# Optimization experiments

Measured on AMD Instinct MI355X. Metric: run time of the kernel, lower is better.

## Reference

```python
import jax, jax.numpy as jnp
import numpy as np

N = 8192          # total nodes in batch
D_IN = 64         # input feature dim
D_H = 64          # hidden dim
D_OUT = 10        # num classes
B = 64            # number of graphs (idx in [0, B))
NUM_ITERS = 5     # power iterations for rs-pool
VALUE_ALPHA = 1.0
EPS = 0.0         # GIN eps (train_eps=False)


def setup_inputs() -> dict:
    key = jax.random.key(0)
    ks = jax.random.split(key, 8)
    x_in = jax.random.normal(ks[0], (N, D_IN), dtype=jnp.float32)
    a = (jax.random.uniform(ks[1], (N, N)) < 0.005).astype(jnp.float32)
    adj = jnp.maximum(a, a.T)
    idx = (jnp.arange(N) // (N // B)).astype(jnp.int32)  # 64 graphs x 128 nodes
    s1 = 1.0 / np.sqrt(D_IN)
    s2 = 1.0 / np.sqrt(D_H)
    W1 = jax.random.uniform(ks[2], (D_IN, D_H), minval=-s1, maxval=s1, dtype=jnp.float32)
    b1 = jax.random.uniform(ks[3], (D_H,), minval=-s1, maxval=s1, dtype=jnp.float32)
    W2 = jax.random.uniform(ks[4], (D_H, D_H), minval=-s2, maxval=s2, dtype=jnp.float32)
    b2 = jax.random.uniform(ks[5], (D_H,), minval=-s2, maxval=s2, dtype=jnp.float32)
    Wl = jax.random.uniform(ks[6], (D_H, D_OUT), minval=-s2, maxval=s2, dtype=jnp.float32)
    bl = jax.random.uniform(ks[7], (D_OUT,), minval=-s2, maxval=s2, dtype=jnp.float32)
    return {"x_in": x_in, "adj": adj, "idx": idx,
            "W1": W1, "b1": b1, "W2": W2, "b2": b2, "Wl": Wl, "bl": bl}


def reference(x_in, adj, idx, W1, b1, W2, b2, Wl, bl):
    n = adj.shape[0]
    A = adj + jnp.eye(n, dtype=adj.dtype)  # self-loops added in forward
    # GINConv: aggregate (A@x + eps*x) then linear + ReLU
    h = jax.nn.relu((A @ x_in + EPS * x_in) @ W1 + b1)   # [N, D_H]
    h = jax.nn.relu((A @ h + EPS * h) @ W2 + b2)         # [N, D_H]

    seg = lambda v: jax.ops.segment_sum(v, idx, num_segments=B)

    # rs-pool: batched power iteration for dominant right singular vector per graph
    vec = seg(h)                                                   # [B, D_H]
    vec = vec / (jnp.linalg.norm(vec, axis=1, keepdims=True) + 1e-8)
    for _ in range(NUM_ITERS):
        y = jnp.sum(h * vec[idx], axis=1, keepdims=True)           # X_g @ v_g, per node
        vec = seg(y * h)                                           # X_g^T (X_g v_g)
        vec = vec / (jnp.linalg.norm(vec, axis=1, keepdims=True) + 1e-8)
    y = jnp.sum(h * vec[idx], axis=1)                              # [N]
    sv = jnp.sqrt(seg(y * y))                                      # ||X_g v_g|| per graph [B]
    pooled = vec * (sv / VALUE_ALPHA)[:, None]                     # [B, D_H]

    out = pooled @ Wl + bl                                         # [B, D_OUT]
    return jax.nn.log_softmax(out, axis=1)
```

## Files before the change

### kernel.cpp

```cpp
#include <hip/hip_runtime.h>
#include <math.h>

#define NN 8192
#define DH 64
#define DOUT 10
#define NG 64
#define NPG 128
#define NITER 5
#define CAP 192
#define CAPW 96

__global__ __launch_bounds__(256) void gin1_fused(
    const float* __restrict__ adj, const float* __restrict__ x,
    const float* __restrict__ W, const float* __restrict__ bias,
    float* __restrict__ h, unsigned short* __restrict__ eidx,
    int* __restrict__ counts)
{
    __shared__ float sW[DH * DH];
    __shared__ float sAccP[4][DH];
    __shared__ float sAccR[DH];
    __shared__ unsigned short sIdx[4][CAPW];
    __shared__ int sCnt[4];

    for (int t = threadIdx.x; t < DH * DH; t += 256) sW[t] = W[t];

    const int wave = threadIdx.x >> 6;
    const int lane = threadIdx.x & 63;
    const int row  = blockIdx.x;

    const float* arow = adj + (size_t)row * NN + wave * 2048;
    const unsigned long long lt = (lane == 63) ? 0x7FFFFFFFFFFFFFFFull
                                               : ((1ull << lane) - 1ull);
    int ec = 0;
    #pragma unroll
    for (int j0 = 0; j0 < 2048; j0 += 256) {
        float4 a4 = *reinterpret_cast<const float4*>(arow + j0 + lane * 4);
        unsigned long long m0 = __ballot(a4.x != 0.0f);
        unsigned long long m1 = __ballot(a4.y != 0.0f);
        unsigned long long m2 = __ballot(a4.z != 0.0f);
        unsigned long long m3 = __ballot(a4.w != 0.0f);
        int pre = __popcll(m0 & lt) + __popcll(m1 & lt) +
                  __popcll(m2 & lt) + __popcll(m3 & lt);
        int pos = ec + pre;
        int jb = wave * 2048 + j0 + 4 * lane;
        if ((m0 >> lane) & 1) sIdx[wave][pos++] = (unsigned short)(jb + 0);
        if ((m1 >> lane) & 1) sIdx[wave][pos++] = (unsigned short)(jb + 1);
        if ((m2 >> lane) & 1) sIdx[wave][pos++] = (unsigned short)(jb + 2);
        if ((m3 >> lane) & 1) sIdx[wave][pos++] = (unsigned short)(jb + 3);
        ec += __popcll(m0) + __popcll(m1) + __popcll(m2) + __popcll(m3);
    }
    if (lane == 0) sCnt[wave] = ec;
    __syncthreads();

    int c0 = sCnt[0], c1 = sCnt[1], c2 = sCnt[2], c3 = sCnt[3];
    int off = (wave > 0 ? c0 : 0) + (wave > 1 ? c1 : 0) + (wave > 2 ? c2 : 0);
    for (int e = lane; e < ec; e += 64)
        eidx[(size_t)row * CAP + off + e] = sIdx[wave][e];
    if (threadIdx.x == 0) counts[row] = c0 + c1 + c2 + c3;

    float acc = (wave == 0) ? x[row * DH + lane] : 0.0f;
    #pragma unroll 4
    for (int e = 0; e < ec; ++e) {
        int j = sIdx[wave][e];
        acc += x[j * DH + lane];
    }
    sAccP[wave][lane] = acc;
    __syncthreads();

    if (wave == 0) {
        float a = sAccP[0][lane] + sAccP[1][lane] + sAccP[2][lane] + sAccP[3][lane];
        sAccR[lane] = a;
        float o = bias[lane];
        #pragma unroll
        for (int k = 0; k < DH; ++k) o += sAccR[k] * sW[k * DH + lane];
        h[row * DH + lane] = fmaxf(o, 0.0f);
    }
}

__global__ __launch_bounds__(256) void gin2_edges(
    const float* __restrict__ x, const unsigned short* __restrict__ eidx,
    const int* __restrict__ counts, const float* __restrict__ W,
    const float* __restrict__ bias, float* __restrict__ out)
{
    __shared__ float sW[DH * DH];
    __shared__ float sAcc[4][DH];
    __shared__ unsigned short sIdx[4][CAP];

    for (int t = threadIdx.x; t < DH * DH; t += 256) sW[t] = W[t];

    const int wave = threadIdx.x >> 6;
    const int lane = threadIdx.x & 63;
    const int row  = (blockIdx.x << 2) + wave;

    const int ec = counts[row];
    for (int e = lane; e < ec; e += 64) sIdx[wave][e] = eidx[(size_t)row * CAP + e];
    __syncthreads();

    float acc = x[row * DH + lane];
    #pragma unroll 4
    for (int e = 0; e < ec; ++e) {
        int j = sIdx[wave][e];
        acc += x[j * DH + lane];
    }

    sAcc[wave][lane] = acc;
    __syncthreads();

    float o = bias[lane];
    #pragma unroll
    for (int k = 0; k < DH; ++k) o += sAcc[wave][k] * sW[k * DH + lane];
    out[row * DH + lane] = fmaxf(o, 0.0f);
}

__global__ __launch_bounds__(256) void rspool_head(
    const float* __restrict__ h, const float* __restrict__ Wl,
    const float* __restrict__ bl, float* __restrict__ out)
{
    __shared__ float sX[NPG * 65];
    __shared__ float sY[NPG];
    __shared__ float sVec[DH];
    __shared__ float sPart[4][DH];
    __shared__ float sPooled[DH];
    __shared__ float sO[DOUT];

    const int g = blockIdx.x;
    const int d = threadIdx.x & 63;
    const int q = threadIdx.x >> 6;

    const float* hg = h + (size_t)g * NPG * DH;
    for (int t = threadIdx.x; t < NPG * DH; t += 256)
        sX[(t >> 6) * 65 + (t & 63)] = hg[t];
    __syncthreads();

    {
        float p = 0.0f;
        for (int i = q * 32; i < q * 32 + 32; ++i) p += sX[i * 65 + d];
        sPart[q][d] = p;
    }
    __syncthreads();
    if (threadIdx.x < 64) {
        float v = sPart[0][d] + sPart[1][d] + sPart[2][d] + sPart[3][d];
        float s = v * v;
        #pragma unroll
        for (int off = 32; off > 0; off >>= 1) s += __shfl_xor(s, off);
        sVec[d] = v / (sqrtf(s) + 1e-8f);
    }
    __syncthreads();

    for (int it = 0; it < NITER; ++it) {
        if (threadIdx.x < NPG) {
            int i = threadIdx.x;
            float yy = 0.0f;
            #pragma unroll
            for (int dd = 0; dd < DH; ++dd) yy += sX[i * 65 + dd] * sVec[dd];
            sY[i] = yy;
        }
        __syncthreads();
        {
            float p = 0.0f;
            for (int i = q * 32; i < q * 32 + 32; ++i) p += sY[i] * sX[i * 65 + d];
            sPart[q][d] = p;
        }
        __syncthreads();
        if (threadIdx.x < 64) {
            float v = sPart[0][d] + sPart[1][d] + sPart[2][d] + sPart[3][d];
            float s = v * v;
            #pragma unroll
            for (int off = 32; off > 0; off >>= 1) s += __shfl_xor(s, off);
            sVec[d] = v / (sqrtf(s) + 1e-8f);
        }
        __syncthreads();
    }

    if (threadIdx.x < NPG) {
        int i = threadIdx.x;
        float yy = 0.0f;
        #pragma unroll
        for (int dd = 0; dd < DH; ++dd) yy += sX[i * 65 + dd] * sVec[dd];
        sY[i] = yy;
    }
    __syncthreads();
    if (threadIdx.x < 64) {
        float s = sY[d] * sY[d] + sY[64 + d] * sY[64 + d];
        #pragma unroll
        for (int off = 32; off > 0; off >>= 1) s += __shfl_xor(s, off);
        float sv = sqrtf(s);
        sPooled[d] = sVec[d] * sv;
    }
    __syncthreads();

    if (threadIdx.x < DOUT) {
        int c = threadIdx.x;
        float o = bl[c];
        #pragma unroll
        for (int dd = 0; dd < DH; ++dd) o += sPooled[dd] * Wl[dd * DOUT + c];
        sO[c] = o;
    }
    __syncthreads();
    if (threadIdx.x < DOUT) {
        int c = threadIdx.x;
        float mx = -INFINITY;
        #pragma unroll
        for (int j = 0; j < DOUT; ++j) mx = fmaxf(mx, sO[j]);
        float se = 0.0f;
        #pragma unroll
        for (int j = 0; j < DOUT; ++j) se += expf(sO[j] - mx);
        out[g * DOUT + c] = sO[c] - mx - logf(se);
    }
}

extern "C" void kernel_launch(void* const* d_in, const int* in_sizes, int n_in,
                              void* d_out, int out_size, void* d_ws, size_t ws_size,
                              hipStream_t stream) {
    const float* x_in = (const float*)d_in[0];
    const float* adj  = (const float*)d_in[1];
    const float* W1 = (const float*)d_in[3];
    const float* b1 = (const float*)d_in[4];
    const float* W2 = (const float*)d_in[5];
    const float* b2 = (const float*)d_in[6];
    const float* Wl = (const float*)d_in[7];
    const float* bl = (const float*)d_in[8];
    float* out = (float*)d_out;

    char* ws = (char*)d_ws;
    float* h1 = (float*)ws;
    float* h2 = h1 + NN * DH;
    int*   counts = (int*)(ws + 4 * 1024 * 1024);
    unsigned short* eidx = (unsigned short*)(ws + 5 * 1024 * 1024);

    gin1_fused<<<NN, 256, 0, stream>>>(adj, x_in, W1, b1, h1, eidx, counts);
    gin2_edges<<<NN / 4, 256, 0, stream>>>(h1, eidx, counts, W2, b2, h2);
    rspool_head<<<NG, 256, 0, stream>>>(h2, Wl, bl, out);
}
```

Baseline: 98.56 us.

## Assign one adjacency row per wave in GIN layer 1 with nontemporal loads

The first GIN kernel now processes four rows per block, each wave scanning a full 8192-wide adjacency row, instead of splitting one row across four waves. This removes the cross-wave count exchange, the partial-sum reduction and the block barriers, and lets every wave run its own linear transform. Adjacency reads use nontemporal loads to avoid polluting the cache with the 256MB streamed matrix. The per-wave __syncthreads after the sAcc write is dropped in both GIN kernels and replaced by wave-local LDS access; this relies on wave-level lockstep ordering, which is a correctness risk.

```diff
diff --git a/kernel.cpp b/kernel.cpp
--- a/kernel.cpp
+++ b/kernel.cpp
@@ -8,7 +8,8 @@
 #define NPG 128
 #define NITER 5
 #define CAP 192
-#define CAPW 96
+
+typedef float f32x4 __attribute__((ext_vector_type(4)));
 
 __global__ __launch_bounds__(256) void gin1_fused(
     const float* __restrict__ adj, const float* __restrict__ x,
@@ -17,24 +18,24 @@
     int* __restrict__ counts)
 {
     __shared__ float sW[DH * DH];
-    __shared__ float sAccP[4][DH];
-    __shared__ float sAccR[DH];
-    __shared__ unsigned short sIdx[4][CAPW];
-    __shared__ int sCnt[4];
+    __shared__ float sAcc[4][DH];
+    __shared__ unsigned short sIdx[4][CAP];
 
     for (int t = threadIdx.x; t < DH * DH; t += 256) sW[t] = W[t];
+    __syncthreads();
 
     const int wave = threadIdx.x >> 6;
     const int lane = threadIdx.x & 63;
-    const int row  = blockIdx.x;
-
-    const float* arow = adj + (size_t)row * NN + wave * 2048;
+    const int row  = (blockIdx.x << 2) + wave;
+
+    const float* arow = adj + (size_t)row * NN;
     const unsigned long long lt = (lane == 63) ? 0x7FFFFFFFFFFFFFFFull
                                                : ((1ull << lane) - 1ull);
     int ec = 0;
-    #pragma unroll
-    for (int j0 = 0; j0 < 2048; j0 += 256) {
-        float4 a4 = *reinterpret_cast<const float4*>(arow + j0 + lane * 4);
+    #pragma unroll 4
+    for (int j0 = 0; j0 < NN; j0 += 256) {
+        f32x4 a4 = __builtin_nontemporal_load(
+            reinterpret_cast<const f32x4*>(arow + j0 + lane * 4));
         unsigned long long m0 = __ballot(a4.x != 0.0f);
         unsigned long long m1 = __ballot(a4.y != 0.0f);
         unsigned long long m2 = __ballot(a4.z != 0.0f);
@@ -42,39 +43,30 @@
         int pre = __popcll(m0 & lt) + __popcll(m1 & lt) +
                   __popcll(m2 & lt) + __popcll(m3 & lt);
         int pos = ec + pre;
-        int jb = wave * 2048 + j0 + 4 * lane;
+        int jb = j0 + 4 * lane;
         if ((m0 >> lane) & 1) sIdx[wave][pos++] = (unsigned short)(jb + 0);
         if ((m1 >> lane) & 1) sIdx[wave][pos++] = (unsigned short)(jb + 1);
         if ((m2 >> lane) & 1) sIdx[wave][pos++] = (unsigned short)(jb + 2);
         if ((m3 >> lane) & 1) sIdx[wave][pos++] = (unsigned short)(jb + 3);
         ec += __popcll(m0) + __popcll(m1) + __popcll(m2) + __popcll(m3);
     }
-    if (lane == 0) sCnt[wave] = ec;
-    __syncthreads();
-
-    int c0 = sCnt[0], c1 = sCnt[1], c2 = sCnt[2], c3 = sCnt[3];
-    int off = (wave > 0 ? c0 : 0) + (wave > 1 ? c1 : 0) + (wave > 2 ? c2 : 0);
+
     for (int e = lane; e < ec; e += 64)
-        eidx[(size_t)row * CAP + off + e] = sIdx[wave][e];
-    if (threadIdx.x == 0) counts[row] = c0 + c1 + c2 + c3;
-
-    float acc = (wave == 0) ? x[row * DH + lane] : 0.0f;
+        eidx[(size_t)row * CAP + e] = sIdx[wave][e];
+    if (lane == 0) counts[row] = ec;
+
+    float acc = x[row * DH + lane];
     #pragma unroll 4
     for (int e = 0; e < ec; ++e) {
         int j = sIdx[wave][e];
         acc += x[j * DH + lane];
     }
-    sAccP[wave][lane] = acc;
-    __syncthreads();
-
-    if (wave == 0) {
-        float a = sAccP[0][lane] + sAccP[1][lane] + sAccP[2][lane] + sAccP[3][lane];
-        sAccR[lane] = a;
-        float o = bias[lane];
-        #pragma unroll
-        for (int k = 0; k < DH; ++k) o += sAccR[k] * sW[k * DH + lane];
-        h[row * DH + lane] = fmaxf(o, 0.0f);
-    }
+
+    sAcc[wave][lane] = acc;
+    float o = bias[lane];
+    #pragma unroll
+    for (int k = 0; k < DH; ++k) o += sAcc[wave][k] * sW[k * DH + lane];
+    h[row * DH + lane] = fmaxf(o, 0.0f);
 }
 
 __global__ __launch_bounds__(256) void gin2_edges(
@@ -104,8 +96,6 @@
     }
 
     sAcc[wave][lane] = acc;
-    __syncthreads();
-
     float o = bias[lane];
     #pragma unroll
     for (int k = 0; k < DH; ++k) o += sAcc[wave][k] * sW[k * DH + lane];
@@ -228,7 +218,7 @@
     int*   counts = (int*)(ws + 4 * 1024 * 1024);
     unsigned short* eidx = (unsigned short*)(ws + 5 * 1024 * 1024);
 
-    gin1_fused<<<NN, 256, 0, stream>>>(adj, x_in, W1, b1, h1, eidx, counts);
+    gin1_fused<<<NN / 4, 256, 0, stream>>>(adj, x_in, W1, b1, h1, eidx, counts);
     gin2_edges<<<NN / 4, 256, 0, stream>>>(h1, eidx, counts, W2, b2, h2);
     rspool_head<<<NG, 256, 0, stream>>>(h2, Wl, bl, out);
 }
```

Result: slower. 108.0 us (+9.6%).
